# Kernel tuning notes

Hardware: AMD Instinct MI355X
Metric: run time of the kernel (lower is better)

Reference implementation:

```python
import jax, jax.numpy as jnp
import numpy as np
import math

D_MODEL = 1024
N_HEADS = 16
HEAD_DIM = D_MODEL // N_HEADS
TOP_FACTOR = 5
B, L = 2, 2048


def setup_inputs() -> dict:
    key = jax.random.key(0)
    ks = jax.random.split(key, 12)
    f = lambda k, shp: jax.random.normal(k, shp, dtype=jnp.float32)
    w = lambda k: f(k, (D_MODEL, D_MODEL)) * 0.02
    return {
        "queries": f(ks[0], (B, L, D_MODEL)),
        "keys": f(ks[1], (B, L, D_MODEL)),
        "values": f(ks[2], (B, L, D_MODEL)),
        "Wq": w(ks[3]), "bq": jnp.zeros((D_MODEL,), jnp.float32),
        "Wk": w(ks[4]), "bk": jnp.zeros((D_MODEL,), jnp.float32),
        "Wv": w(ks[5]), "bv": jnp.zeros((D_MODEL,), jnp.float32),
        "Wo": w(ks[6]), "bo": jnp.zeros((D_MODEL,), jnp.float32),
    }


def reference(queries, keys, values, Wq, bq, Wk, bk, Wv, bv, Wo, bo):
    Bq, L_q, _ = queries.shape
    L_k = keys.shape[1]
    H, D = N_HEADS, HEAD_DIM

    def proj(x, W, b, Lx):
        return (x @ W.T + b).reshape(Bq, Lx, H, D).transpose(0, 2, 1, 3)  # (B,H,L,D)

    q = proj(queries, Wq, bq, L_q)
    k = proj(keys, Wk, bk, L_k)
    v = proj(values, Wv, bv, L_k)

    # Normalized QK score pass for query ranking
    q_norm = q / jnp.linalg.norm(q, axis=-1, keepdims=True)
    k_norm = k / jnp.linalg.norm(k, axis=-1, keepdims=True)
    scores_all = jnp.einsum("bhqd,bhkd->bhqk", q_norm, k_norm)  # (B,H,Lq,Lk)
    mean_scores = scores_all.mean(axis=-1)                        # (B,H,Lq)

    u = max(1, L_q // TOP_FACTOR)
    _, top_idx = jax.lax.top_k(mean_scores, u)                    # (B,H,u)

    # Gather selected queries and run dense attention on them
    q_sel = jnp.take_along_axis(q, top_idx[..., None], axis=2)    # (B,H,u,D)
    scores = jnp.einsum("bhud,bhkd->bhuk", q_sel, k) / math.sqrt(D)
    attn = jax.nn.softmax(scores, axis=-1)
    ctx_sel = jnp.einsum("bhuk,bhkd->bhud", attn, v)              # (B,H,u,D)

    # Scatter back into zero context tensor
    bidx = jnp.arange(Bq)[:, None, None]
    hidx = jnp.arange(H)[None, :, None]
    context = jnp.zeros((Bq, H, L_q, D), dtype=queries.dtype)
    context = context.at[bidx, hidx, top_idx].set(ctx_sel)

    out = context.transpose(0, 2, 1, 3).reshape(Bq, L_q, H * D)
    return out @ Wo.T + bo
```

## Files before the change

### kernel.cpp

```cpp
#include <hip/hip_runtime.h>
#include <math.h>

#define NB 2
#define NL 2048
#define NH 16
#define ND 64
#define NDM 1024
#define NU 409
#define NUP 416
#define NBH (NB*NH)
#define NROWS (NB*NL)
#define NRTOT (NB*NH*NL)
#define MTOT (NBH*NUP)

typedef short bf16x8 __attribute__((ext_vector_type(8)));
typedef short bf16x4 __attribute__((ext_vector_type(4)));
typedef float f32x4  __attribute__((ext_vector_type(4)));

__device__ __forceinline__ short f2bf(float x) {
  unsigned u = __float_as_uint(x);
  return (short)((u + 0x7FFFu + ((u >> 16) & 1u)) >> 16);
}
__device__ __forceinline__ float bf2f(short s) {
  return __uint_as_float(((unsigned)(unsigned short)s) << 16);
}

__device__ __forceinline__ void gload16(const short* g, short* l) {
  __builtin_amdgcn_global_load_lds(
      (const __attribute__((address_space(1))) void*)g,
      (__attribute__((address_space(3))) void*)l, 16, 0, 0);
}

struct SplitDesc { const float* in; short* a; short* b; short* c; int nc; int nblk; };
struct SplitArgs { SplitDesc d[7]; };

__global__ __launch_bounds__(256) void msplit_k(SplitArgs args) {
  const SplitDesc d = args.d[blockIdx.z];
  if ((int)blockIdx.x >= d.nblk) return;
  const size_t i = (size_t)blockIdx.x * 256 + threadIdx.x;
  const float4 x0 = ((const float4*)d.in)[2*i];
  const float4 x1 = ((const float4*)d.in)[2*i + 1];
  float x[8] = {x0.x,x0.y,x0.z,x0.w, x1.x,x1.y,x1.z,x1.w};
  bf16x8 va, vb;
  #pragma unroll
  for (int j = 0; j < 8; ++j) {
    const short A = f2bf(x[j]);
    va[j] = A;
    vb[j] = f2bf(x[j] - bf2f(A));
  }
  *(bf16x8*)(d.a + 8*i) = va;
  if (d.nc >= 2) *(bf16x8*)(d.b + 8*i) = vb;
}

struct GemmDesc {
  const short* X[2];
  const short* W[2];
  const float* bias;
  float* C;
  short* KbfVt;
  double* kpart;
  int sbeg, send;
  int mode;
};
struct GemmArgs { GemmDesc d[3]; };

__global__ __launch_bounds__(256, 3) void gemm_mega_k(GemmArgs args) {
  __shared__ short As[128*64];
  __shared__ short Bs[128*64];
  const int fid = blockIdx.x;
  const int xcd = fid & 7, jd = fid >> 3;
  const int s = jd % 3, jj = jd / 3;
  const int tile = (xcd << 5) + jj;
  const int bx = tile & 7, by = tile >> 3;
  const GemmDesc d = args.d[s];
  const int tid = threadIdx.x;
  const int wv = tid >> 6, L = tid & 63;
  const int lr = L & 15, lg = L >> 4;
  const int n0 = bx << 7, m0 = by << 7;
  const int wm = (wv >> 1) << 6, wn = (wv & 1) << 6;
  const int sr = tid >> 3, ssl = tid & 7;

  f32x4 acc[4][4];
  #pragma unroll
  for (int i = 0; i < 4; ++i)
    #pragma unroll
    for (int j = 0; j < 4; ++j) acc[i][j] = (f32x4){0.f,0.f,0.f,0.f};

  for (int step = d.sbeg; step < d.send; ++step) {
    const int c = step >> 4, kk = (step & 15) << 6;
    const short *Xg, *Wg;
    switch (c) {
      case 0:  Xg = d.X[0]; Wg = d.W[0]; break;
      case 1:  Xg = d.X[0]; Wg = d.W[1]; break;
      default: Xg = d.X[1]; Wg = d.W[0]; break;
    }
    #pragma unroll
    for (int j = 0; j < 4; ++j) {
      const int row = (j << 5) + sr;
      const int slot = (ssl ^ (row & 7)) << 3;
      gload16(Xg + (size_t)(m0 + row) * NDM + kk + slot, As + (j << 11) + (tid << 3));
      gload16(Wg + (size_t)(n0 + row) * NDM + kk + slot, Bs + (j << 11) + (tid << 3));
    }
    __syncthreads();
    #pragma unroll
    for (int c2 = 0; c2 < 2; ++c2) {
      const int sl = (((c2 << 2) + lg) ^ (lr & 7)) << 3;
      bf16x8 af[4], bfr[4];
      #pragma unroll
      for (int t = 0; t < 4; ++t) {
        af[t]  = *(const bf16x8*)(As + ((wm + (t << 4) + lr) << 6) + sl);
        bfr[t] = *(const bf16x8*)(Bs + ((wn + (t << 4) + lr) << 6) + sl);
      }
      #pragma unroll
      for (int mt = 0; mt < 4; ++mt)
        #pragma unroll
        for (int nt = 0; nt < 4; ++nt)
          acc[mt][nt] = __builtin_amdgcn_mfma_f32_16x16x32_bf16(bfr[nt], af[mt], acc[mt][nt], 0, 0, 0);
    }
    __syncthreads();
  }

  if (d.mode == 1) {
    const int b2 = by >> 4;
    const int hw = (bx << 1) + (wv & 1);
    const int bh = (b2 << 4) + hw;
    const int seg = ((by & 15) << 1) + (wv >> 1);
    float kv[4][4][4];
    double inv[4];
    #pragma unroll
    for (int mt = 0; mt < 4; ++mt) {
      float ss = 0.f;
      #pragma unroll
      for (int nt = 0; nt < 4; ++nt) {
        const int n = n0 + wn + (nt << 4) + (lg << 2);
        const float4 b4 = *(const float4*)(d.bias + n);
        kv[mt][nt][0] = acc[mt][nt][0] + b4.x;
        kv[mt][nt][1] = acc[mt][nt][1] + b4.y;
        kv[mt][nt][2] = acc[mt][nt][2] + b4.z;
        kv[mt][nt][3] = acc[mt][nt][3] + b4.w;
        #pragma unroll
        for (int j = 0; j < 4; ++j) ss += kv[mt][nt][j] * kv[mt][nt][j];
      }
      ss += __shfl_xor(ss, 16);
      ss += __shfl_xor(ss, 32);
      inv[mt] = 1.0 / sqrt((double)ss);
    }
    #pragma unroll
    for (int mt = 0; mt < 4; ++mt) {
      const int l = (m0 + wm + (mt << 4) + lr) & (NL - 1);
      short* kp = d.KbfVt + (((size_t)bh * NL + l) << 6);
      #pragma unroll
      for (int nt = 0; nt < 4; ++nt) {
        const int dd = (nt << 4) + (lg << 2);
        bf16x4 o;
        #pragma unroll
        for (int j = 0; j < 4; ++j) o[j] = f2bf(kv[mt][nt][j]);
        *(bf16x4*)(kp + dd) = o;
      }
    }
    #pragma unroll
    for (int nt = 0; nt < 4; ++nt) {
      double p[4];
      #pragma unroll
      for (int j = 0; j < 4; ++j) {
        p[j] = 0.0;
        #pragma unroll
        for (int mt = 0; mt < 4; ++mt) p[j] += (double)kv[mt][nt][j] * inv[mt];
        p[j] += __shfl_xor(p[j], 1);
        p[j] += __shfl_xor(p[j], 2);
        p[j] += __shfl_xor(p[j], 4);
        p[j] += __shfl_xor(p[j], 8);
      }
      if (lr == 0) {
        const int dd = (nt << 4) + (lg << 2);
        double* kp = d.kpart + ((((size_t)bh << 5) + seg) << 6) + dd;
        kp[0] = p[0]; kp[1] = p[1]; kp[2] = p[2]; kp[3] = p[3];
      }
    }
  } else if (d.mode == 2) {
    #pragma unroll
    for (int nt = 0; nt < 4; ++nt) {
      const int nl = wn + (nt << 4) + (lg << 2);
      const float4 b4 = *(const float4*)(d.bias + n0 + nl);
      #pragma unroll
      for (int j2 = 0; j2 < 4; ++j2) {
        const int row = nl + j2;
        short* Tp = (row & 64) ? Bs : As;
        const int rr = row & 63;
        const float bj = (j2 == 0) ? b4.x : (j2 == 1) ? b4.y : (j2 == 2) ? b4.z : b4.w;
        const int sw = (row & 7) << 3;
        #pragma unroll
        for (int mt = 0; mt < 4; ++mt) {
          const int m = wm + (mt << 4) + lr;
          Tp[rr * 128 + (m ^ sw)] = f2bf(acc[mt][nt][j2] + bj);
        }
      }
    }
    __syncthreads();
    {
      const int r = tid >> 1, seg2 = tid & 1;
      const short* Tp = (r & 64) ? Bs : As;
      const int rr = r & 63, sw = (r & 7) << 3;
      const int ngl = n0 + r, h = ngl >> 6, dd2 = ngl & 63;
      const int bb = m0 >> 11, ll = m0 & (NL - 1);
      short* dst = d.KbfVt + (((size_t)((((bb << 4) + h) << 6) + dd2)) << 11) + ll + (seg2 << 6);
      #pragma unroll
      for (int i = 0; i < 8; ++i)
        *(bf16x8*)(dst + (i << 3)) =
            *(const bf16x8*)(Tp + rr * 128 + (((seg2 << 6) + (i << 3)) ^ sw));
    }
  } else {
    #pragma unroll
    for (int nt = 0; nt < 4; ++nt) {
      const int n = n0 + wn + (nt << 4) + (lg << 2);
      const float4 b4 = *(const float4*)(d.bias + n);
      #pragma unroll
      for (int mt = 0; mt < 4; ++mt) {
        f32x4 a = acc[mt][nt];
        a[0] += b4.x; a[1] += b4.y; a[2] += b4.z; a[3] += b4.w;
        const int m = m0 + wm + (mt << 4) + lr;
        const int bb = m >> 11, ll = m & (NL - 1);
        const int hh = n >> 6, dd = n & 63;
        *(f32x4*)(d.C + (((size_t)(bb*NH + hh)*NL + ll) << 6) + dd) = a;
      }
    }
  }
}

__global__ __launch_bounds__(256) void wtilde_k(const float* __restrict__ Wq,
                                                const float* __restrict__ bq,
                                                const double* __restrict__ kpart,
                                                float* __restrict__ wt,
                                                double* __restrict__ s0) {
  __shared__ double kb[64];
  const int bh = blockIdx.x, h = bh & 15;
  const int tid = threadIdx.x;
  if (tid < 64) {
    double s = 0.0;
    #pragma unroll
    for (int seg = 0; seg < 32; ++seg)
      s += kpart[((((size_t)bh << 5) + seg) << 6) + tid];
    kb[tid] = s * (1.0 / NL);
  }
  __syncthreads();
  const int j = (blockIdx.y << 8) + tid;
  double a = 0.0;
  #pragma unroll 8
  for (int d = 0; d < 64; ++d)
    a += (double)Wq[(((size_t)((h << 6) + d)) << 10) + j] * kb[d];
  wt[((size_t)bh << 10) + j] = (float)a;
  if (blockIdx.y == 0 && tid < 64) {
    double p = (double)bq[(h << 6) + tid] * kb[tid];
    #pragma unroll
    for (int off = 32; off > 0; off >>= 1) p += __shfl_xor(p, off);
    if (tid == 0) s0[bh] = p;
  }
}

__global__ __launch_bounds__(256) void dotqms_k(const float* __restrict__ x,
                                                const float* __restrict__ Qb,
                                                const float* __restrict__ wt,
                                                const double* __restrict__ s0,
                                                float* __restrict__ ms) {
  __shared__ float xs[1024];
  __shared__ double sm[16][16];
  __shared__ double sq[16][16];
  const int r = blockIdx.x, b = r >> 11, l = r & (NL - 1);
  const int tid = threadIdx.x;
  ((float4*)xs)[tid] = ((const float4*)(x + ((size_t)r << 10)))[tid];
  __syncthreads();
  const int h = tid >> 4, t = tid & 15;
  const float* w = wt + ((size_t)((b << 4) + h) << 10);
  double a = 0.0;
  #pragma unroll 8
  for (int i = 0; i < 64; ++i) {
    const int j = t + (i << 4);
    a += (double)xs[j] * (double)w[j];
  }
  sm[h][t] = a;
  const float4 qv = *(const float4*)(Qb + (((size_t)((b << 4) + h) * NL + l) << 6) + (t << 2));
  sq[h][t] = (double)qv.x*qv.x + (double)qv.y*qv.y + (double)qv.z*qv.z + (double)qv.w*qv.w;
  __syncthreads();
  if (tid < 16) {
    double s = 0.0, ssq = 0.0;
    #pragma unroll
    for (int t2 = 0; t2 < 16; ++t2) { s += sm[tid][t2]; ssq += sq[tid][t2]; }
    ms[(((size_t)(b << 4) + tid) << 11) + l] = (float)((s + s0[(b << 4) + tid]) / sqrt(ssq));
  }
}

__global__ __launch_bounds__(256) void select_rank_k(const float* __restrict__ ms,
                                                     int* __restrict__ sel,
                                                     int* __restrict__ invsel) {
  __shared__ unsigned long long keys[NL];
  const int bh = blockIdx.x >> 3, seg = blockIdx.x & 7;
  const int tid = threadIdx.x;
  for (int l = tid; l < NL; l += 256) {
    unsigned u = __float_as_uint(ms[(size_t)bh * NL + l]);
    u = (u & 0x80000000u) ? ~u : (u | 0x80000000u);
    keys[l] = ((unsigned long long)u << 32) | (unsigned)(NL - 1 - l);
  }
  __syncthreads();
  const int r = (seg << 8) + tid;
  const unsigned long long mine = keys[r];
  int cnt = 0;
  #pragma unroll 8
  for (int l = 0; l < NL; ++l) cnt += (keys[l] > mine) ? 1 : 0;
  if (cnt < NU) sel[bh*NU + cnt] = r;
  invsel[(size_t)bh * NL + r] = (cnt < NU) ? cnt : NU;
}

__global__ __launch_bounds__(512) void fattn_k(const float* __restrict__ Qb,
                                               const int* __restrict__ sel,
                                               const short* __restrict__ Kbf,
                                               const short* __restrict__ Vt,
                                               short* __restrict__ Ca,
                                               short* __restrict__ Cb) {
  __shared__ short S[32*2048];
  __shared__ float inv_s[32];
  int bid = blockIdx.x;
  bid = (bid & 7) * 52 + (bid >> 3);
  const int m0 = bid << 5;
  const int bh = m0 / NUP;
  const int u0 = m0 - bh * NUP;
  const int tid = threadIdx.x;
  const int w = tid >> 6, L = tid & 63;
  const int lr = L & 15, lg = L >> 4;

  bf16x8 qf[2][2];
  #pragma unroll
  for (int mt = 0; mt < 2; ++mt) {
    const int u = u0 + mt*16 + lr;
    const int lq = (u < NU) ? sel[bh*NU + u] : 0;
    const float* qp = Qb + (((size_t)bh*NL + lq) << 6) + lg*8;
    const float4 q0 = *(const float4*)qp;
    const float4 q1 = *(const float4*)(qp + 4);
    const float4 q2 = *(const float4*)(qp + 32);
    const float4 q3 = *(const float4*)(qp + 36);
    qf[mt][0][0]=f2bf(q0.x); qf[mt][0][1]=f2bf(q0.y); qf[mt][0][2]=f2bf(q0.z); qf[mt][0][3]=f2bf(q0.w);
    qf[mt][0][4]=f2bf(q1.x); qf[mt][0][5]=f2bf(q1.y); qf[mt][0][6]=f2bf(q1.z); qf[mt][0][7]=f2bf(q1.w);
    qf[mt][1][0]=f2bf(q2.x); qf[mt][1][1]=f2bf(q2.y); qf[mt][1][2]=f2bf(q2.z); qf[mt][1][3]=f2bf(q2.w);
    qf[mt][1][4]=f2bf(q3.x); qf[mt][1][5]=f2bf(q3.y); qf[mt][1][6]=f2bf(q3.z); qf[mt][1][7]=f2bf(q3.w);
  }
  const int nb = w << 8;
  const short* kb0 = Kbf + (((size_t)bh*NL + nb + lr) << 6) + lg*8;
  #pragma unroll 2
  for (int nt = 0; nt < 16; ++nt) {
    const short* kp = kb0 + ((size_t)nt << 10);
    const bf16x8 kf0 = *(const bf16x8*)kp;
    const bf16x8 kf1 = *(const bf16x8*)(kp + 32);
    #pragma unroll
    for (int mt = 0; mt < 2; ++mt) {
      f32x4 a = {0.f,0.f,0.f,0.f};
      a = __builtin_amdgcn_mfma_f32_16x16x32_bf16(kf0, qf[mt][0], a, 0, 0, 0);
      a = __builtin_amdgcn_mfma_f32_16x16x32_bf16(kf1, qf[mt][1], a, 0, 0, 0);
      const int m = mt*16 + lr;
      bf16x4 o;
      #pragma unroll
      for (int r = 0; r < 4; ++r) o[r] = f2bf(a[r] * 0.125f);
      const int byteoff = (m << 12) + ((((nb + nt*16 + lg*4) << 1)) ^ ((m & 7) << 4));
      *(bf16x4*)((char*)S + byteoff) = o;
    }
  }
  __syncthreads();

  #pragma unroll
  for (int j = 0; j < 4; ++j) {
    const int R = (w << 2) + j;
    char* rowp = (char*)S + (R << 12);
    const int sw = (R & 7) << 4;
    bf16x8 v[4];
    #pragma unroll
    for (int i = 0; i < 4; ++i)
      v[i] = *(const bf16x8*)(rowp + (((L << 6) + (i << 4)) ^ sw));
    float f[32];
    #pragma unroll
    for (int i = 0; i < 4; ++i)
      #pragma unroll
      for (int e = 0; e < 8; ++e) f[i*8+e] = bf2f(v[i][e]);
    float mx = f[0];
    #pragma unroll
    for (int i = 1; i < 32; ++i) mx = fmaxf(mx, f[i]);
    #pragma unroll
    for (int off = 32; off > 0; off >>= 1) mx = fmaxf(mx, __shfl_xor(mx, off));
    float sum = 0.f;
    #pragma unroll
    for (int i = 0; i < 32; ++i) { f[i] = __expf(f[i] - mx); sum += f[i]; }
    #pragma unroll
    for (int off = 32; off > 0; off >>= 1) sum += __shfl_xor(sum, off);
    bf16x8 p[4];
    #pragma unroll
    for (int i = 0; i < 4; ++i)
      #pragma unroll
      for (int e = 0; e < 8; ++e) p[i][e] = f2bf(f[i*8+e]);
    #pragma unroll
    for (int i = 0; i < 4; ++i)
      *(bf16x8*)(rowp + (((L << 6) + (i << 4)) ^ sw)) = p[i];
    if (L == 0) inv_s[R] = 1.f / sum;
  }
  __syncthreads();

  {
    const int mt = w & 1, dt = w >> 1;
    const int m = mt*16 + lr;
    const char* arow = (const char*)S + (m << 12);
    const int sw = (m & 7) << 4;
    const short* vrow = Vt + (((size_t)bh*ND + dt*16 + lr) << 11) + lg*8;
    f32x4 acc0 = {0.f,0.f,0.f,0.f}, acc1 = {0.f,0.f,0.f,0.f};
    for (int k0 = 0; k0 < NL; k0 += 64) {
      const bf16x8 p0 = *(const bf16x8*)(arow + ((((k0 + lg*8) << 1)) ^ sw));
      const bf16x8 p1 = *(const bf16x8*)(arow + ((((k0 + 32 + lg*8) << 1)) ^ sw));
      const bf16x8 v0 = *(const bf16x8*)(vrow + k0);
      const bf16x8 v1 = *(const bf16x8*)(vrow + k0 + 32);
      acc0 = __builtin_amdgcn_mfma_f32_16x16x32_bf16(p0, v0, acc0, 0, 0, 0);
      acc1 = __builtin_amdgcn_mfma_f32_16x16x32_bf16(p1, v1, acc1, 0, 0, 0);
    }
    const int ub = u0 + mt*16 + (lg << 2);
    #pragma unroll
    for (int r = 0; r < 4; ++r) {
      float val = (acc0[r] + acc1[r]) * inv_s[mt*16 + (lg << 2) + r];
      if (ub + r >= NU) val = 0.f;
      const size_t off = (((size_t)m0 + mt*16 + (lg << 2) + r) << 6) + dt*16 + lr;
      const short A = f2bf(val);
      Ca[off] = A;
      Cb[off] = f2bf(val - bf2f(A));
    }
  }
}

struct OselArgs {
  const short* Xa; const short* Xb;
  const short* Wa; const short* Wb;
  float* C0; float* C1; float* C2;
  const int* invsel;
};

__global__ __launch_bounds__(256, 3) void gemm_osel_k(OselArgs ar) {
  __shared__ short As[128*64];
  __shared__ short Bs[128*64];
  __shared__ int utbl[2048];
  const int fid = blockIdx.x;
  const int xcd = fid & 7, jd = fid >> 3;
  const int zi = jd % 3;
  const int o = (xcd << 5) + (jd / 3);
  const int bx = o & 7, by = o >> 3;
  const int sbeg = zi << 4, send = sbeg + 16;
  float* C = (zi == 0) ? ar.C0 : (zi == 1) ? ar.C1 : ar.C2;
  const int tid = threadIdx.x;
  const int wv = tid >> 6, L = tid & 63;
  const int lr = L & 15, lg = L >> 4;
  const int n0 = bx << 7, m0 = by << 7;
  const int wm = (wv >> 1) << 6, wn = (wv & 1) << 6;
  const int sr = tid >> 3, ssl = tid & 7;
  const int b2 = by >> 4;

  #pragma unroll
  for (int e = 0; e < 8; ++e) {
    const int idx = (tid << 3) + e;
    const int row = idx >> 4, h = idx & 15;
    utbl[idx] = ar.invsel[((((size_t)b2 << 4) + h) << 11) + ((m0 + row) & (NL - 1))];
  }
  __syncthreads();

  f32x4 acc[4][4];
  #pragma unroll
  for (int i = 0; i < 4; ++i)
    #pragma unroll
    for (int j = 0; j < 4; ++j) acc[i][j] = (f32x4){0.f,0.f,0.f,0.f};

  for (int step = sbeg; step < send; ++step) {
    const int c = step >> 4, kk = (step & 15) << 6;
    const short* Wg = (c == 1) ? ar.Wb : ar.Wa;
    const short* Xs = (c == 2) ? ar.Xb : ar.Xa;
    #pragma unroll
    for (int j = 0; j < 4; ++j) {
      const int row = (j << 5) + sr;
      const int slot = (ssl ^ (row & 7)) << 3;
      const int h = step & 15;
      const int u = utbl[(row << 4) + h];
      gload16(Xs + (((size_t)((b2 << 4) + h) * NUP + u) << 6) + slot,
              As + (j << 11) + (tid << 3));
      gload16(Wg + (size_t)(n0 + row) * NDM + kk + slot, Bs + (j << 11) + (tid << 3));
    }
    __syncthreads();
    #pragma unroll
    for (int c2 = 0; c2 < 2; ++c2) {
      const int sl = (((c2 << 2) + lg) ^ (lr & 7)) << 3;
      bf16x8 af[4], bfr[4];
      #pragma unroll
      for (int t = 0; t < 4; ++t) {
        af[t]  = *(const bf16x8*)(As + ((wm + (t << 4) + lr) << 6) + sl);
        bfr[t] = *(const bf16x8*)(Bs + ((wn + (t << 4) + lr) << 6) + sl);
      }
      #pragma unroll
      for (int mt = 0; mt < 4; ++mt)
        #pragma unroll
        for (int nt = 0; nt < 4; ++nt)
          acc[mt][nt] = __builtin_amdgcn_mfma_f32_16x16x32_bf16(bfr[nt], af[mt], acc[mt][nt], 0, 0, 0);
    }
    __syncthreads();
  }

  #pragma unroll
  for (int nt = 0; nt < 4; ++nt) {
    const int n = n0 + wn + (nt << 4) + (lg << 2);
    #pragma unroll
    for (int mt = 0; mt < 4; ++mt) {
      const int m = m0 + wm + (mt << 4) + lr;
      *(f32x4*)(C + ((size_t)m << 10) + n) = acc[mt][nt];
    }
  }
}

__global__ __launch_bounds__(256) void oadd_k(float* __restrict__ out,
                                              const float* __restrict__ P1,
                                              const float* __restrict__ P2,
                                              const float* __restrict__ bo) {
  const size_t i4 = (size_t)blockIdx.x * 256 + threadIdx.x;
  const size_t i = i4 << 2;
  float4 a = *(float4*)(out + i);
  const float4 b = *(const float4*)(P1 + i);
  const float4 c = *(const float4*)(P2 + i);
  const float4 d = *(const float4*)(bo + ((i4 & 255) << 2));
  a.x += b.x + c.x + d.x; a.y += b.y + c.y + d.y;
  a.z += b.z + c.z + d.z; a.w += b.w + c.w + d.w;
  *(float4*)(out + i) = a;
}

extern "C" void kernel_launch(void* const* d_in, const int* in_sizes, int n_in,
                              void* d_out, int out_size, void* d_ws, size_t ws_size,
                              hipStream_t stream)
{
  (void)in_sizes; (void)n_in; (void)out_size; (void)ws_size;
  const float* queries = (const float*)d_in[0];
  const float* keys    = (const float*)d_in[1];
  const float* values  = (const float*)d_in[2];
  const float* Wq = (const float*)d_in[3];  const float* bq = (const float*)d_in[4];
  const float* Wk = (const float*)d_in[5];  const float* bk = (const float*)d_in[6];
  const float* Wv = (const float*)d_in[7];  const float* bv = (const float*)d_in[8];
  const float* Wo = (const float*)d_in[9];  const float* bo = (const float*)d_in[10];
  float* out = (float*)d_out;

  char* base = (char*)d_ws;
  #define MB(x) ((size_t)(x) << 20)

  short* Qa   = (short*)(base + MB(0));
  short* Qb2  = (short*)(base + MB(8));
  short* Ka   = (short*)(base + MB(16));
  short* Kb2  = (short*)(base + MB(24));
  short* Kbf  = (short*)(base + MB(32));
  short* Vbf  = (short*)(base + MB(40));
  float* Qb   = (float*)(base + MB(48));
  short* Vt   = (short*)(base + MB(64));
  short* Wqa  = (short*)(base + MB(72));
  short* Wqb  = (short*)(base + MB(74));
  short* Wka  = (short*)(base + MB(76));
  short* Wkb  = (short*)(base + MB(78));
  short* Wvbf = (short*)(base + MB(80));
  short* Woa  = (short*)(base + MB(82));
  short* Wob  = (short*)(base + MB(84));
  char* sm = base + MB(86);
  double* kpart  = (double*)sm;  sm += 524288;
  float*  wt     = (float*)sm;   sm += 131072;
  double* s0     = (double*)sm;  sm += 512;
  float*  msb    = (float*)sm;   sm += 262144;
  int*    sel    = (int*)sm;     sm += 65536;
  int*    invsel = (int*)sm;     sm += 262144;

  short* CselA = Vbf;
  short* CselB = (short*)(base + MB(42));
  float* P1o   = Qb;
  float* P2o   = (float*)Ka;

  {
    SplitArgs a;
    a.d[0] = {queries, Qa, Qb2, nullptr, 2, 2048};
    a.d[1] = {keys,    Ka, Kb2, nullptr, 2, 2048};
    a.d[2] = {values,  Vbf, nullptr, nullptr, 1, 2048};
    a.d[3] = {Wq, Wqa, Wqb, nullptr, 2, 512};
    a.d[4] = {Wk, Wka, Wkb, nullptr, 2, 512};
    a.d[5] = {Wv, Wvbf, nullptr, nullptr, 1, 512};
    a.d[6] = {Wo, Woa, Wob, nullptr, 2, 512};
    msplit_k<<<dim3(2048,1,7), 256, 0, stream>>>(a);
  }
  {
    GemmArgs g;
    g.d[0] = {{Qa,Qb2},   {Wqa,Wqb},   bq, Qb,      nullptr, nullptr, 0, 48, 0};
    g.d[1] = {{Ka,Kb2},   {Wka,Wkb},   bk, nullptr, Kbf,     kpart,   0, 48, 1};
    g.d[2] = {{Vbf,Vbf},  {Wvbf,Wvbf}, bv, nullptr, Vt,      nullptr, 0, 16, 2};
    gemm_mega_k<<<768, 256, 0, stream>>>(g);
  }
  wtilde_k<<<dim3(NBH,4), 256, 0, stream>>>(Wq, bq, kpart, wt, s0);
  dotqms_k<<<NROWS, 256, 0, stream>>>(queries, Qb, wt, s0, msb);
  select_rank_k<<<NBH*8, 256, 0, stream>>>(msb, sel, invsel);

  fattn_k<<<MTOT/32, 512, 0, stream>>>(Qb, sel, Kbf, Vt, CselA, CselB);

  {
    OselArgs oa = {CselA, CselB, Woa, Wob, out, P1o, P2o, invsel};
    gemm_osel_k<<<768, 256, 0, stream>>>(oa);
  }
  oadd_k<<<4096, 256, 0, stream>>>(out, P1o, P2o, bo);
}
```

Baseline: 237.4 us.

## Emit bf16 Q with fused row norms and drop split-bf16 context in output GEMM

The Q projection epilogue now writes bf16 Q directly and computes per-row squared norms in the GEMM, so the fp32 Q buffer is no longer stored or reread. The ranking kernel reads the precomputed norms and the attention kernel loads bf16 Q without converting. The attention output is stored as a single bf16 value instead of a hi/lo split, which removes one of the three error-compensation passes in the output GEMM. That GEMM's split-K is rebalanced into four 8-step chunks over 1024 blocks, and the final add sums one extra partial. The cost is lower precision in the attention context, with some risk to accuracy.

```diff
diff --git a/kernel.cpp b/kernel.cpp
--- a/kernel.cpp
+++ b/kernel.cpp
@@ -56,9 +56,9 @@
   const short* X[2];
   const short* W[2];
   const float* bias;
-  float* C;
   short* KbfVt;
   double* kpart;
+  float* sq;
   int sbeg, send;
   int mode;
 };
@@ -177,7 +177,40 @@
         kp[0] = p[0]; kp[1] = p[1]; kp[2] = p[2]; kp[3] = p[3];
       }
     }
-  } else if (d.mode == 2) {
+  } else if (d.mode == 3) {
+    const int b2 = by >> 4;
+    const int hw = (bx << 1) + (wv & 1);
+    const int bh = (b2 << 4) + hw;
+    #pragma unroll
+    for (int mt = 0; mt < 4; ++mt) {
+      float kv[4][4];
+      float ss = 0.f;
+      #pragma unroll
+      for (int nt = 0; nt < 4; ++nt) {
+        const int n = n0 + wn + (nt << 4) + (lg << 2);
+        const float4 b4 = *(const float4*)(d.bias + n);
+        kv[nt][0] = acc[mt][nt][0] + b4.x;
+        kv[nt][1] = acc[mt][nt][1] + b4.y;
+        kv[nt][2] = acc[mt][nt][2] + b4.z;
+        kv[nt][3] = acc[mt][nt][3] + b4.w;
+        #pragma unroll
+        for (int j = 0; j < 4; ++j) ss += kv[nt][j] * kv[nt][j];
+      }
+      ss += __shfl_xor(ss, 16);
+      ss += __shfl_xor(ss, 32);
+      const int l = (m0 + wm + (mt << 4) + lr) & (NL - 1);
+      if (lg == 0) d.sq[((size_t)bh << 11) + l] = ss;
+      short* qp = d.KbfVt + (((size_t)bh * NL + l) << 6);
+      #pragma unroll
+      for (int nt = 0; nt < 4; ++nt) {
+        const int dd = (nt << 4) + (lg << 2);
+        bf16x4 o;
+        #pragma unroll
+        for (int j = 0; j < 4; ++j) o[j] = f2bf(kv[nt][j]);
+        *(bf16x4*)(qp + dd) = o;
+      }
+    }
+  } else {
     #pragma unroll
     for (int nt = 0; nt < 4; ++nt) {
       const int nl = wn + (nt << 4) + (lg << 2);
@@ -208,21 +241,6 @@
       for (int i = 0; i < 8; ++i)
         *(bf16x8*)(dst + (i << 3)) =
             *(const bf16x8*)(Tp + rr * 128 + (((seg2 << 6) + (i << 3)) ^ sw));
-    }
-  } else {
-    #pragma unroll
-    for (int nt = 0; nt < 4; ++nt) {
-      const int n = n0 + wn + (nt << 4) + (lg << 2);
-      const float4 b4 = *(const float4*)(d.bias + n);
-      #pragma unroll
-      for (int mt = 0; mt < 4; ++mt) {
-        f32x4 a = acc[mt][nt];
-        a[0] += b4.x; a[1] += b4.y; a[2] += b4.z; a[3] += b4.w;
-        const int m = m0 + wm + (mt << 4) + lr;
-        const int bb = m >> 11, ll = m & (NL - 1);
-        const int hh = n >> 6, dd = n & 63;
-        *(f32x4*)(d.C + (((size_t)(bb*NH + hh)*NL + ll) << 6) + dd) = a;
-      }
     }
   }
 }
@@ -258,13 +276,12 @@
 }
 
 __global__ __launch_bounds__(256) void dotqms_k(const float* __restrict__ x,
-                                                const float* __restrict__ Qb,
+                                                const float* __restrict__ sqv,
                                                 const float* __restrict__ wt,
                                                 const double* __restrict__ s0,
                                                 float* __restrict__ ms) {
   __shared__ float xs[1024];
   __shared__ double sm[16][16];
-  __shared__ double sq[16][16];
   const int r = blockIdx.x, b = r >> 11, l = r & (NL - 1);
   const int tid = threadIdx.x;
   ((float4*)xs)[tid] = ((const float4*)(x + ((size_t)r << 10)))[tid];
@@ -278,14 +295,13 @@
     a += (double)xs[j] * (double)w[j];
   }
   sm[h][t] = a;
-  const float4 qv = *(const float4*)(Qb + (((size_t)((b << 4) + h) * NL + l) << 6) + (t << 2));
-  sq[h][t] = (double)qv.x*qv.x + (double)qv.y*qv.y + (double)qv.z*qv.z + (double)qv.w*qv.w;
   __syncthreads();
   if (tid < 16) {
-    double s = 0.0, ssq = 0.0;
-    #pragma unroll
-    for (int t2 = 0; t2 < 16; ++t2) { s += sm[tid][t2]; ssq += sq[tid][t2]; }
-    ms[(((size_t)(b << 4) + tid) << 11) + l] = (float)((s + s0[(b << 4) + tid]) / sqrt(ssq));
+    double s = 0.0;
+    #pragma unroll
+    for (int t2 = 0; t2 < 16; ++t2) s += sm[tid][t2];
+    const size_t ro = (((size_t)(b << 4) + tid) << 11) + l;
+    ms[ro] = (float)((s + s0[(b << 4) + tid]) / sqrt((double)sqv[ro]));
   }
 }
 
@@ -310,12 +326,11 @@
   invsel[(size_t)bh * NL + r] = (cnt < NU) ? cnt : NU;
 }
 
-__global__ __launch_bounds__(512) void fattn_k(const float* __restrict__ Qb,
+__global__ __launch_bounds__(512) void fattn_k(const short* __restrict__ Qbf,
                                                const int* __restrict__ sel,
                                                const short* __restrict__ Kbf,
                                                const short* __restrict__ Vt,
-                                               short* __restrict__ Ca,
-                                               short* __restrict__ Cb) {
+                                               short* __restrict__ Csel) {
   __shared__ short S[32*2048];
   __shared__ float inv_s[32];
   int bid = blockIdx.x;
@@ -332,15 +347,9 @@
   for (int mt = 0; mt < 2; ++mt) {
     const int u = u0 + mt*16 + lr;
     const int lq = (u < NU) ? sel[bh*NU + u] : 0;
-    const float* qp = Qb + (((size_t)bh*NL + lq) << 6) + lg*8;
-    const float4 q0 = *(const float4*)qp;
-    const float4 q1 = *(const float4*)(qp + 4);
-    const float4 q2 = *(const float4*)(qp + 32);
-    const float4 q3 = *(const float4*)(qp + 36);
-    qf[mt][0][0]=f2bf(q0.x); qf[mt][0][1]=f2bf(q0.y); qf[mt][0][2]=f2bf(q0.z); qf[mt][0][3]=f2bf(q0.w);
-    qf[mt][0][4]=f2bf(q1.x); qf[mt][0][5]=f2bf(q1.y); qf[mt][0][6]=f2bf(q1.z); qf[mt][0][7]=f2bf(q1.w);
-    qf[mt][1][0]=f2bf(q2.x); qf[mt][1][1]=f2bf(q2.y); qf[mt][1][2]=f2bf(q2.z); qf[mt][1][3]=f2bf(q2.w);
-    qf[mt][1][4]=f2bf(q3.x); qf[mt][1][5]=f2bf(q3.y); qf[mt][1][6]=f2bf(q3.z); qf[mt][1][7]=f2bf(q3.w);
+    const short* qp = Qbf + (((size_t)bh*NL + lq) << 6) + lg*8;
+    qf[mt][0] = *(const bf16x8*)qp;
+    qf[mt][1] = *(const bf16x8*)(qp + 32);
   }
   const int nb = w << 8;
   const short* kb0 = Kbf + (((size_t)bh*NL + nb + lr) << 6) + lg*8;
@@ -421,17 +430,15 @@
       float val = (acc0[r] + acc1[r]) * inv_s[mt*16 + (lg << 2) + r];
       if (ub + r >= NU) val = 0.f;
       const size_t off = (((size_t)m0 + mt*16 + (lg << 2) + r) << 6) + dt*16 + lr;
-      const short A = f2bf(val);
-      Ca[off] = A;
-      Cb[off] = f2bf(val - bf2f(A));
+      Csel[off] = f2bf(val);
     }
   }
 }
 
 struct OselArgs {
-  const short* Xa; const short* Xb;
+  const short* X;
   const short* Wa; const short* Wb;
-  float* C0; float* C1; float* C2;
+  float* C0; float* C1; float* C2; float* C3;
   const int* invsel;
 };
 
@@ -441,11 +448,11 @@
   __shared__ int utbl[2048];
   const int fid = blockIdx.x;
   const int xcd = fid & 7, jd = fid >> 3;
-  const int zi = jd % 3;
-  const int o = (xcd << 5) + (jd / 3);
+  const int zi = jd & 3;
+  const int o = (xcd << 5) + (jd >> 2);
   const int bx = o & 7, by = o >> 3;
-  const int sbeg = zi << 4, send = sbeg + 16;
-  float* C = (zi == 0) ? ar.C0 : (zi == 1) ? ar.C1 : ar.C2;
+  const int sbeg = zi << 3, send = sbeg + 8;
+  float* C = (zi == 0) ? ar.C0 : (zi == 1) ? ar.C1 : (zi == 2) ? ar.C2 : ar.C3;
   const int tid = threadIdx.x;
   const int wv = tid >> 6, L = tid & 63;
   const int lr = L & 15, lg = L >> 4;
@@ -470,15 +477,14 @@
 
   for (int step = sbeg; step < send; ++step) {
     const int c = step >> 4, kk = (step & 15) << 6;
-    const short* Wg = (c == 1) ? ar.Wb : ar.Wa;
-    const short* Xs = (c == 2) ? ar.Xb : ar.Xa;
+    const short* Wg = c ? ar.Wb : ar.Wa;
     #pragma unroll
     for (int j = 0; j < 4; ++j) {
       const int row = (j << 5) + sr;
       const int slot = (ssl ^ (row & 7)) << 3;
       const int h = step & 15;
       const int u = utbl[(row << 4) + h];
-      gload16(Xs + (((size_t)((b2 << 4) + h) * NUP + u) << 6) + slot,
+      gload16(ar.X + (((size_t)((b2 << 4) + h) * NUP + u) << 6) + slot,
               As + (j << 11) + (tid << 3));
       gload16(Wg + (size_t)(n0 + row) * NDM + kk + slot, Bs + (j << 11) + (tid << 3));
     }
@@ -515,15 +521,17 @@
 __global__ __launch_bounds__(256) void oadd_k(float* __restrict__ out,
                                               const float* __restrict__ P1,
                                               const float* __restrict__ P2,
+                                              const float* __restrict__ P3,
                                               const float* __restrict__ bo) {
   const size_t i4 = (size_t)blockIdx.x * 256 + threadIdx.x;
   const size_t i = i4 << 2;
   float4 a = *(float4*)(out + i);
   const float4 b = *(const float4*)(P1 + i);
   const float4 c = *(const float4*)(P2 + i);
+  const float4 e = *(const float4*)(P3 + i);
   const float4 d = *(const float4*)(bo + ((i4 & 255) << 2));
-  a.x += b.x + c.x + d.x; a.y += b.y + c.y + d.y;
-  a.z += b.z + c.z + d.z; a.w += b.w + c.w + d.w;
+  a.x += b.x + c.x + e.x + d.x; a.y += b.y + c.y + e.y + d.y;
+  a.z += b.z + c.z + e.z + d.z; a.w += b.w + c.w + e.w + d.w;
   *(float4*)(out + i) = a;
 }
 
@@ -550,27 +558,28 @@
   short* Kb2  = (short*)(base + MB(24));
   short* Kbf  = (short*)(base + MB(32));
   short* Vbf  = (short*)(base + MB(40));
-  float* Qb   = (float*)(base + MB(48));
-  short* Vt   = (short*)(base + MB(64));
-  short* Wqa  = (short*)(base + MB(72));
-  short* Wqb  = (short*)(base + MB(74));
-  short* Wka  = (short*)(base + MB(76));
-  short* Wkb  = (short*)(base + MB(78));
-  short* Wvbf = (short*)(base + MB(80));
-  short* Woa  = (short*)(base + MB(82));
-  short* Wob  = (short*)(base + MB(84));
-  char* sm = base + MB(86);
+  short* Qbf  = (short*)(base + MB(48));
+  float* P1o  = (float*)(base + MB(56));
+  short* Vt   = (short*)(base + MB(72));
+  short* Wqa  = (short*)(base + MB(80));
+  short* Wqb  = (short*)(base + MB(82));
+  short* Wka  = (short*)(base + MB(84));
+  short* Wkb  = (short*)(base + MB(86));
+  short* Wvbf = (short*)(base + MB(88));
+  short* Woa  = (short*)(base + MB(90));
+  short* Wob  = (short*)(base + MB(92));
+  char* sm = base + MB(94);
   double* kpart  = (double*)sm;  sm += 524288;
   float*  wt     = (float*)sm;   sm += 131072;
   double* s0     = (double*)sm;  sm += 512;
+  float*  sqv    = (float*)sm;   sm += 262144;
   float*  msb    = (float*)sm;   sm += 262144;
   int*    sel    = (int*)sm;     sm += 65536;
   int*    invsel = (int*)sm;     sm += 262144;
 
-  short* CselA = Vbf;
-  short* CselB = (short*)(base + MB(42));
-  float* P1o   = Qb;
-  float* P2o   = (float*)Ka;
+  short* Csel = Vbf;
+  float* P2o  = (float*)Ka;
+  float* P3o  = (float*)Qa;
 
   {
     SplitArgs a;
@@ -585,20 +594,20 @@
   }
   {
     GemmArgs g;
-    g.d[0] = {{Qa,Qb2},   {Wqa,Wqb},   bq, Qb,      nullptr, nullptr, 0, 48, 0};
-    g.d[1] = {{Ka,Kb2},   {Wka,Wkb},   bk, nullptr, Kbf,     kpart,   0, 48, 1};
-    g.d[2] = {{Vbf,Vbf},  {Wvbf,Wvbf}, bv, nullptr, Vt,      nullptr, 0, 16, 2};
+    g.d[0] = {{Qa,Qb2},  {Wqa,Wqb},   bq, Qbf, nullptr, sqv,     0, 48, 3};
+    g.d[1] = {{Ka,Kb2},  {Wka,Wkb},   bk, Kbf, kpart,   nullptr, 0, 48, 1};
+    g.d[2] = {{Vbf,Vbf}, {Wvbf,Wvbf}, bv, Vt,  nullptr, nullptr, 0, 16, 2};
     gemm_mega_k<<<768, 256, 0, stream>>>(g);
   }
   wtilde_k<<<dim3(NBH,4), 256, 0, stream>>>(Wq, bq, kpart, wt, s0);
-  dotqms_k<<<NROWS, 256, 0, stream>>>(queries, Qb, wt, s0, msb);
+  dotqms_k<<<NROWS, 256, 0, stream>>>(queries, sqv, wt, s0, msb);
   select_rank_k<<<NBH*8, 256, 0, stream>>>(msb, sel, invsel);
 
-  fattn_k<<<MTOT/32, 512, 0, stream>>>(Qb, sel, Kbf, Vt, CselA, CselB);
+  fattn_k<<<MTOT/32, 512, 0, stream>>>(Qbf, sel, Kbf, Vt, Csel);
 
   {
-    OselArgs oa = {CselA, CselB, Woa, Wob, out, P1o, P2o, invsel};
-    gemm_osel_k<<<768, 256, 0, stream>>>(oa);
-  }
-  oadd_k<<<4096, 256, 0, stream>>>(out, P1o, P2o, bo);
-}
+    OselArgs oa = {Csel, Woa, Wob, out, P1o, P2o, P3o, invsel};
+    gemm_osel_k<<<1024, 256, 0, stream>>>(oa);
+  }
+  oadd_k<<<4096, 256, 0, stream>>>(out, P1o, P2o, P3o, bo);
+}
```

After: 233.9 us. No clear change (-1.5%).
